# Kernel tuning notes

Hardware: AMD Instinct MI355X
Metric: run time of the kernel (lower is better)

## Reference

```python
import jax, jax.numpy as jnp
import numpy as np

NUM_SCALES = 5


def _window_params(T, num_scales):
    window_sizes = [max(4, int(T // 2 ** i)) for i in range(num_scales)]
    strides = [w // 2 for w in window_sizes]
    return window_sizes, strides


def setup_inputs() -> dict:
    key = jax.random.key(0)
    B, C, T = 64, 64, 4096
    x = jax.random.normal(key, (B, C, T), dtype=jnp.float32)
    return {"x": x}


def reference(x):
    # x: [B, C, T]
    B, C, T = x.shape
    window_sizes, strides = _window_params(T, NUM_SCALES)
    outs = []
    for w, s in zip(window_sizes, strides):
        n_windows = max(1, (T - w) // s + 1)
        starts = jnp.arange(n_windows) * s            # [n]
        idx = starts[:, None] + jnp.arange(w)          # [n, w]
        win = x[:, :, idx]                             # [B, C, n, w]
        d = jnp.diff(win, axis=-1)                     # [B, C, n, w-1]
        # zero-crossing count of the first difference
        zc = jnp.sum(d[..., :-1] * d[..., 1:] < 0, axis=-1).astype(jnp.float32)  # [B, C, n]
        numerator = jnp.float32(np.log10(w))
        denominator = numerator + jnp.log10(jnp.float32(w) / (w + 0.4 * zc))
        outs.append(numerator / denominator)           # petrosian FD per window
    return jnp.concatenate(outs, axis=2)               # [B, C, sum(n_windows)]
```

## Files before the change

kernel.cpp:

```cpp
#include <hip/hip_runtime.h>
#include <math.h>


constexpr int TLEN = 4096;
constexpr int NW   = 57;

__global__ __launch_bounds__(256) void pfd_kernel(const float* __restrict__ x,
                                                  float* __restrict__ out) {
    __shared__ float xs[TLEN];
    __shared__ int   wc[16][4];
    __shared__ int   pseg[33];

    const int tid = threadIdx.x;
    const int row = blockIdx.x;
    const size_t base = (size_t)row * TLEN;

    const float4* xv = reinterpret_cast<const float4*>(x + base);
    float4* sv = reinterpret_cast<float4*>(xs);
#pragma unroll
    for (int m = 0; m < 4; ++m)
        sv[tid + 256 * m] = xv[tid + 256 * m];
    __syncthreads();

    const int wave = tid >> 6;
    const int lane = tid & 63;

#pragma unroll
    for (int k = 0; k < 16; ++k) {
        const int i = (k << 8) + tid;
        bool pred = false;
        if (i <= TLEN - 3) {
            const float a = xs[i];
            const float b = xs[i + 1];
            const float c = xs[i + 2];
            const float d0 = b - a;
            const float d1 = c - b;
            pred = (d0 * d1 < 0.0f);
        }
        const unsigned long long m = __ballot(pred);
        if (lane == 0) wc[k][wave] = __popcll(m);
    }
    __syncthreads();

    if (tid == 0) {
        int acc = 0;
        pseg[0] = 0;
#pragma unroll
        for (int k = 0; k < 16; ++k) {
            acc += wc[k][0] + wc[k][1];
            pseg[2 * k + 1] = acc;
            acc += wc[k][2] + wc[k][3];
            pseg[2 * k + 2] = acc;
        }
    }
    __syncthreads();

    if (tid < NW) {
        int scale, off;
        if (tid < 1)       { scale = 0; off = 0;  }
        else if (tid < 4)  { scale = 1; off = 1;  }
        else if (tid < 11) { scale = 2; off = 4;  }
        else if (tid < 26) { scale = 3; off = 11; }
        else               { scale = 4; off = 26; }
        const int w      = TLEN >> scale;
        const int stride = w >> 1;
        const int s      = (tid - off) * stride;
        const int e      = s + w;

        int zc = pseg[e >> 7] - pseg[s >> 7];
        if (e < TLEN) {
            const float x0 = xs[e - 2], x1 = xs[e - 1], x2 = xs[e], x3 = xs[e + 1];
            const float d0 = x1 - x0, d1 = x2 - x1, d2 = x3 - x2;
            zc -= (d0 * d1 < 0.0f) ? 1 : 0;
            zc -= (d1 * d2 < 0.0f) ? 1 : 0;
        }

        const float wf  = (float)w;
        const float num = log10f(wf);
        const float den = num + log10f(wf / (wf + 0.4f * (float)zc));
        out[(size_t)row * NW + tid] = num / den;
    }
}

extern "C" void kernel_launch(void* const* d_in, const int* in_sizes, int n_in,
                              void* d_out, int out_size, void* d_ws, size_t ws_size,
                              hipStream_t stream) {
    const float* x = (const float*)d_in[0];
    float* out = (float*)d_out;
    const int rows = in_sizes[0] / TLEN;
    pfd_kernel<<<dim3(rows), dim3(256), 0, stream>>>(x, out);
}
```

Measured before the change: 89.74 us.

## Compute zero-crossings directly from float4 registers with wave shuffles, dropping shared staging

Removes the 16 KB shared-memory staging of each row. Each thread now loads a float4 from global memory and gets its neighbour's values through a wave shuffle, so it can evaluate four crossing predicates in registers. Ballot counts are split into 32-lane halves so the 128-element segment prefix sums stay the same. This cuts LDS traffic and one barrier and raises occupancy, but lane 63 and the window-boundary fixups now read global memory directly.

```diff
diff --git a/kernel.cpp b/kernel.cpp
--- a/kernel.cpp
+++ b/kernel.cpp
@@ -7,38 +7,60 @@
 
 __global__ __launch_bounds__(256) void pfd_kernel(const float* __restrict__ x,
                                                   float* __restrict__ out) {
-    __shared__ float xs[TLEN];
-    __shared__ int   wc[16][4];
-    __shared__ int   pseg[33];
+    __shared__ int wc[32];
+    __shared__ int pseg[33];
 
-    const int tid = threadIdx.x;
-    const int row = blockIdx.x;
-    const size_t base = (size_t)row * TLEN;
-
-    const float4* xv = reinterpret_cast<const float4*>(x + base);
-    float4* sv = reinterpret_cast<float4*>(xs);
-#pragma unroll
-    for (int m = 0; m < 4; ++m)
-        sv[tid + 256 * m] = xv[tid + 256 * m];
-    __syncthreads();
-
+    const int tid  = threadIdx.x;
+    const int row  = blockIdx.x;
     const int wave = tid >> 6;
     const int lane = tid & 63;
+    const size_t base = (size_t)row * TLEN;
+    const float* __restrict__ g = x + base;
+    const float4* __restrict__ gv = reinterpret_cast<const float4*>(g);
 
 #pragma unroll
-    for (int k = 0; k < 16; ++k) {
-        const int i = (k << 8) + tid;
-        bool pred = false;
-        if (i <= TLEN - 3) {
-            const float a = xs[i];
-            const float b = xs[i + 1];
-            const float c = xs[i + 2];
-            const float d0 = b - a;
-            const float d1 = c - b;
-            pred = (d0 * d1 < 0.0f);
+    for (int k = 0; k < 4; ++k) {
+        const int q    = (k << 8) + tid;
+        const int fidx = q << 2;
+        const float4 v = gv[q];
+
+        float nx = __shfl_down(v.x, 1);
+        float ny = __shfl_down(v.y, 1);
+        if (lane == 63) {
+            if (fidx + 4 < TLEN) {
+                nx = g[fidx + 4];
+                ny = g[fidx + 5];
+            } else {
+                nx = 0.0f; ny = 0.0f;
+            }
         }
-        const unsigned long long m = __ballot(pred);
-        if (lane == 0) wc[k][wave] = __popcll(m);
+
+        const float d0 = v.y - v.x;
+        const float d1 = v.z - v.y;
+        const float d2 = v.w - v.z;
+        const float d3 = nx  - v.w;
+        const float d4 = ny  - nx;
+
+        const bool p0 = (d0 * d1 < 0.0f) && (fidx     <= TLEN - 3);
+        const bool p1 = (d1 * d2 < 0.0f) && (fidx + 1 <= TLEN - 3);
+        const bool p2 = (d2 * d3 < 0.0f) && (fidx + 2 <= TLEN - 3);
+        const bool p3 = (d3 * d4 < 0.0f) && (fidx + 3 <= TLEN - 3);
+
+        const unsigned long long m0 = __ballot(p0);
+        const unsigned long long m1 = __ballot(p1);
+        const unsigned long long m2 = __ballot(p2);
+        const unsigned long long m3 = __ballot(p3);
+
+        if (lane == 0) {
+            const unsigned int lo = 0xffffffffu;
+            const int cntA = __popcll(m0 & lo) + __popcll(m1 & lo)
+                           + __popcll(m2 & lo) + __popcll(m3 & lo);
+            const int cntB = __popcll(m0 >> 32) + __popcll(m1 >> 32)
+                           + __popcll(m2 >> 32) + __popcll(m3 >> 32);
+            const int sA = (k << 3) + (wave << 1);
+            wc[sA]     = cntA;
+            wc[sA + 1] = cntB;
+        }
     }
     __syncthreads();
 
@@ -46,11 +68,9 @@
         int acc = 0;
         pseg[0] = 0;
 #pragma unroll
-        for (int k = 0; k < 16; ++k) {
-            acc += wc[k][0] + wc[k][1];
-            pseg[2 * k + 1] = acc;
-            acc += wc[k][2] + wc[k][3];
-            pseg[2 * k + 2] = acc;
+        for (int i = 0; i < 32; ++i) {
+            acc += wc[i];
+            pseg[i + 1] = acc;
         }
     }
     __syncthreads();
@@ -69,7 +89,7 @@
 
         int zc = pseg[e >> 7] - pseg[s >> 7];
         if (e < TLEN) {
-            const float x0 = xs[e - 2], x1 = xs[e - 1], x2 = xs[e], x3 = xs[e + 1];
+            const float x0 = g[e - 2], x1 = g[e - 1], x2 = g[e], x3 = g[e + 1];
             const float d0 = x1 - x0, d1 = x2 - x1, d2 = x3 - x2;
             zc -= (d0 * d1 < 0.0f) ? 1 : 0;
             zc -= (d1 * d2 < 0.0f) ? 1 : 0;
```

Result: slower. 93.07 us (+3.7%).
